# Kernel optimization log

Measured on AMD Instinct MI355X. Metric: run time of the kernel, lower is better.

Reference implementation:

```python
import jax, jax.numpy as jnp
import numpy as np

N, E, G = 10000, 160000, 64     # nodes, edges, graphs in batch
T, F_IN, F_OUT, L = 5, 75, 15, 4  # towers, per-tower in (divide_input=False), per-tower out, conv layers
AVG_DEG_LOG = float(np.log(17.0))  # stand-in for PyG histogram stat (source deg=zeros -> NaN)
BN_EPS = 1e-5
STD_EPS = 1e-5


def _u(key, shape):
    fi, fo = shape[-2], shape[-1]
    lim = float(np.sqrt(6.0 / (fi + fo)))
    return jax.random.uniform(key, shape, jnp.float32, -lim, lim)


def setup_inputs():
    key = jax.random.key(0)
    k = iter(jax.random.split(key, 24))
    inp = {}
    inp["x"] = jax.random.randint(next(k), (N, 2), 0, 21)
    inp["edge_index"] = jax.random.randint(next(k), (2, E), 0, N)
    inp["edge_attr"] = jax.random.randint(next(k), (E, 2), 0, 4)
    inp["batch"] = jnp.sort(jax.random.randint(next(k), (N,), 0, G))
    inp["node_emb"] = jax.random.normal(next(k), (21, 75), jnp.float32)
    inp["edge_emb"] = jax.random.normal(next(k), (4, 25), jnp.float32)
    inp["pre_lin_W"] = _u(next(k), (150, 75)); inp["pre_lin_b"] = jnp.zeros((75,), jnp.float32)
    inp["edge_enc_W"] = _u(next(k), (L, 50, F_IN)); inp["edge_enc_b"] = jnp.zeros((L, F_IN), jnp.float32)
    inp["pre_W"] = _u(next(k), (L, T, 3 * F_IN, F_IN)); inp["pre_b"] = jnp.zeros((L, T, F_IN), jnp.float32)
    inp["post_W"] = _u(next(k), (L, T, 13 * F_IN, F_OUT)); inp["post_b"] = jnp.zeros((L, T, F_OUT), jnp.float32)
    inp["lin_W"] = _u(next(k), (L, T * F_OUT, 75)); inp["lin_b"] = jnp.zeros((L, 75), jnp.float32)
    inp["bn_g"] = jnp.ones((L, 75), jnp.float32); inp["bn_b"] = jnp.zeros((L, 75), jnp.float32)
    inp["mlp_W1"] = _u(next(k), (75, 50)); inp["mlp_b1"] = jnp.zeros((50,), jnp.float32)
    inp["mlp_W2"] = _u(next(k), (50, 25)); inp["mlp_b2"] = jnp.zeros((25,), jnp.float32)
    inp["mlp_W3"] = _u(next(k), (25, 1)); inp["mlp_b3"] = jnp.zeros((1,), jnp.float32)
    return inp


def _forward(x, edge_index, edge_attr, batch, node_emb, edge_emb, pre_lin_W, pre_lin_b,
             edge_enc_W, edge_enc_b, pre_W, pre_b, post_W, post_b, lin_W, lin_b,
             bn_g, bn_b, mlp_W1, mlp_b1, mlp_W2, mlp_b2, mlp_W3, mlp_b3):
    # node / edge embeddings -> features
    h = node_emb[x].reshape(N, 150) @ pre_lin_W + pre_lin_b          # [N,75]
    ea = edge_emb[edge_attr].reshape(E, 50)                           # [E,50]
    src, dst = edge_index[0], edge_index[1]  # messages flow src -> dst (x_j=src, x_i=dst)

    cnt = jax.ops.segment_sum(jnp.ones((E,), jnp.float32), dst, num_segments=N)  # in-degree [N]
    deg = jnp.maximum(cnt, 1.0)[:, None, None]
    log_deg = jnp.log(jnp.maximum(cnt, 1.0) + 1.0)[:, None, None]
    amp = log_deg / AVG_DEG_LOG
    att = AVG_DEG_LOG / log_deg
    has = (cnt > 0)[:, None, None]

    for l in range(L):
        e = ea @ edge_enc_W[l] + edge_enc_b[l]                        # [E,75]
        m_in = jnp.concatenate([h[dst], h[src], e], axis=-1)          # [E,225]
        msgs = jnp.einsum('ec,tcf->etf', m_in, pre_W[l]) + pre_b[l]   # [E,T,75]
        s = jax.ops.segment_sum(msgs, dst, num_segments=N)
        mean = s / deg
        mean_sq = jax.ops.segment_sum(msgs * msgs, dst, num_segments=N) / deg
        std = jnp.sqrt(jax.nn.relu(mean_sq - mean * mean) + STD_EPS)
        mn = jnp.where(has, jax.ops.segment_min(msgs, dst, num_segments=N), 0.0)
        mx = jnp.where(has, jax.ops.segment_max(msgs, dst, num_segments=N), 0.0)
        agg = jnp.concatenate([mean, mn, mx, std], axis=-1)           # [N,T,300]
        scaled = jnp.concatenate([agg, agg * amp, agg * att], axis=-1)  # [N,T,900]
        out = jnp.concatenate([jnp.broadcast_to(h[:, None, :], (N, T, F_IN)), scaled], axis=-1)  # [N,T,975]
        post = jnp.einsum('ntc,tcf->ntf', out, post_W[l]) + post_b[l]  # [N,T,15]
        hc = post.reshape(N, T * F_OUT) @ lin_W[l] + lin_b[l]          # [N,75]
        mu = hc.mean(axis=0)
        var = hc.var(axis=0)  # biased, matches BatchNorm1d training mode
        h = jax.nn.relu((hc - mu) / jnp.sqrt(var + BN_EPS) * bn_g[l] + bn_b[l])

    g = jax.ops.segment_sum(h, batch, num_segments=G)                 # global_add_pool [G,75]
    g = jax.nn.relu(g @ mlp_W1 + mlp_b1)
    g = jax.nn.relu(g @ mlp_W2 + mlp_b2)
    return g @ mlp_W3 + mlp_b3                                        # [G,1]


def reference(x, edge_index, edge_attr, batch, node_emb, edge_emb, pre_lin_W, pre_lin_b,
              edge_enc_W, edge_enc_b, pre_W, pre_b, post_W, post_b, lin_W, lin_b,
              bn_g, bn_b, mlp_W1, mlp_b1, mlp_W2, mlp_b2, mlp_W3, mlp_b3):
    return _forward(x, edge_index, edge_attr, batch, node_emb, edge_emb, pre_lin_W, pre_lin_b,
                    edge_enc_W, edge_enc_b, pre_W, pre_b, post_W, post_b, lin_W, lin_b,
                    bn_g, bn_b, mlp_W1, mlp_b1, mlp_W2, mlp_b2, mlp_W3, mlp_b3)
```

## Files before the change

kernel.cpp:

```cpp
#include <hip/hip_runtime.h>
#include <hip/hip_bf16.h>
#include <math.h>

#define NN 10000
#define NE 160000
#define NG 64
#define NT 5
#define NL 4
#define ADL 2.833213344056216f

#define OFF_H      0
#define OFF_HC     750000
#define OFF_P      1500000
#define OFF_Q      5250000
#define OFF_AGG    9000000
#define OFF_RLUT4  16500000
#define OFF_INVDEG 24006000
#define OFF_AMP    24016000
#define OFF_ATT    24026000
#define OFF_STATS  24036000
#define OFF_GPOOL  24040000
#define OFF_INT    24118960

typedef __attribute__((ext_vector_type(2))) unsigned int uv2;

__device__ __forceinline__ float bf2f(__hip_bfloat16 v){ return __bfloat162float(v); }

__global__ void k_zero_cnt(int* cnt){
    int i = blockIdx.x*256 + threadIdx.x;
    if (i < NN) cnt[i] = 0;
}

__global__ __launch_bounds__(256) void k_h0(const int* __restrict__ x,
        const float* __restrict__ node_emb, const float* __restrict__ plW,
        const float* __restrict__ plb, float* __restrict__ h){
    __shared__ float s_emb[21*75];
    __shared__ float s_W[150*75];
    __shared__ float s_b[75];
    int tid = threadIdx.x;
    for (int i = tid; i < 21*75; i += 256) s_emb[i] = node_emb[i];
    for (int i = tid; i < 150*75; i += 256) s_W[i] = plW[i];
    if (tid < 75) s_b[tid] = plb[tid];
    __syncthreads();
    for (int out = blockIdx.x*256 + tid; out < NN*75; out += gridDim.x*256){
        int n = out / 75, f = out - n*75;
        int x0 = x[2*n], x1 = x[2*n+1];
        float acc = s_b[f];
        const float* e0 = s_emb + x0*75;
        const float* e1 = s_emb + x1*75;
        #pragma unroll 5
        for (int k = 0; k < 75; k++)
            acc += e0[k]*s_W[k*75+f] + e1[k]*s_W[(75+k)*75+f];
        h[out] = acc;
    }
}

__global__ void k_hist(const int* __restrict__ ei, int* __restrict__ cnt){
    int e = blockIdx.x*256 + threadIdx.x;
    if (e < NE) atomicAdd(&cnt[ei[NE + e]], 1);
}

__global__ __launch_bounds__(1024) void k_scan(const int* __restrict__ cnt,
        int* __restrict__ eoff, float* __restrict__ invdeg,
        float* __restrict__ amp, float* __restrict__ att,
        int* __restrict__ cursor){
    __shared__ int wsum[16];
    int tid = threadIdx.x;
    int base = tid*10;
    int v[10];
    int s = 0;
    #pragma unroll
    for (int i = 0; i < 10; i++){
        int n = base + i;
        int c = (n < NN) ? cnt[n] : 0;
        v[i] = s;
        s += c;
    }
    int lane = tid & 63;
    int wave = tid >> 6;
    int inc = s;
    #pragma unroll
    for (int off = 1; off < 64; off <<= 1){
        int t = __shfl_up(inc, off);
        if (lane >= off) inc += t;
    }
    if (lane == 63) wsum[wave] = inc;
    __syncthreads();
    if (tid == 0){
        int acc = 0;
        #pragma unroll
        for (int w = 0; w < 16; w++){ int t = wsum[w]; wsum[w] = acc; acc += t; }
        eoff[0] = 0;
    }
    __syncthreads();
    int ex = inc - s + wsum[wave];
    #pragma unroll
    for (int i = 0; i < 10; i++){
        int n = base + i;
        if (n < NN){
            int c = cnt[n];
            int start = ex + v[i];
            eoff[n+1] = start + c;
            cursor[n] = start;
            float cf = (float)c;
            float dg = cf < 1.f ? 1.f : cf;
            invdeg[n] = 1.f / dg;
            float ld = logf(dg + 1.f);
            amp[n] = ld / ADL;
            att[n] = ADL / ld;
        }
    }
}

__global__ void k_scatter(const int* __restrict__ ei, const int* __restrict__ ea,
        int* __restrict__ cursor, int* __restrict__ esrc, int* __restrict__ ecombo){
    int e = blockIdx.x*256 + threadIdx.x;
    if (e >= NE) return;
    int src = ei[e], dst = ei[NE + e];
    int pos = atomicAdd(&cursor[dst], 1);
    esrc[pos] = src;
    ecombo[pos] = ea[2*e]*4 + ea[2*e+1];
}

__global__ __launch_bounds__(384) void k_rlut4(
        const float* __restrict__ preW, const float* __restrict__ preb,
        const float* __restrict__ edge_emb, const float* __restrict__ encW,
        const float* __restrict__ encb, float* __restrict__ rlut_all){
    __shared__ float smem[10675];
    int tid = threadIdx.x;
    int t = blockIdx.x;
    int l = blockIdx.y;
    float* s_encW = smem;
    float* s_ev   = smem + 3750;
    float* s_wc   = smem + 4950;
    float* s_ee   = smem + 10575;
    for (int i = tid; i < 3750; i += 384) s_encW[i] = encW[(size_t)l*3750 + i];
    for (int i = tid; i < 100; i += 384) s_ee[i] = edge_emb[i];
    const float* wcsrc = preW + (((size_t)(l*NT + t))*225 + 150)*75;
    for (int i = tid; i < 5625; i += 384) s_wc[i] = wcsrc[i];
    __syncthreads();
    for (int task = tid; task < 1200; task += 384){
        int b = task/75, m = task - 75*b;
        int a0 = b >> 2, a1 = b & 3;
        float s = encb[l*75 + m];
        for (int k = 0; k < 25; k++)
            s += s_ee[a0*25+k]*s_encW[k*75+m] + s_ee[a1*25+k]*s_encW[(25+k)*75+m];
        s_ev[task] = s;
    }
    __syncthreads();
    for (int task = tid; task < 1200; task += 384){
        int b = task/75, f = task - 75*b;
        float r = preb[((size_t)l*NT + t)*75 + f];
        const float* ev = s_ev + b*75;
        #pragma unroll 5
        for (int m = 0; m < 75; m++) r += ev[m]*s_wc[m*75 + f];
        rlut_all[(size_t)l*6000 + b*375 + t*75 + f] = r;
    }
}

__global__ __launch_bounds__(256, 4) void k_pq(float* __restrict__ h,
        const float* __restrict__ hc, const float* __restrict__ bng,
        const float* __restrict__ bnb,
        const float* __restrict__ preW,
        int l, __hip_bfloat16* __restrict__ P, __hip_bfloat16* __restrict__ Q,
        const float* __restrict__ stats_all){
    __shared__ float s_h[64*76];
    __shared__ float s_w[76*64];
    int tid = threadIdx.x;
    int base_n = blockIdx.x*64;
    int tx = tid & 15;
    int ty = tid >> 4;

    if (l == 0){
        for (int idx = tid; idx < 64*76; idx += 256){
            int i = idx/76, m = idx - 76*i;
            int n = base_n + i;
            s_h[idx] = (m < 75 && n < NN) ? h[(size_t)n*75 + m] : 0.f;
        }
    } else {
        const float* stats_rd = stats_all + ((l + 1) & 1)*192;
        int lp = l - 1;
        for (int idx = tid; idx < 64*76; idx += 256){
            int i = idx/76, m = idx - 76*i;
            int n = base_n + i;
            float v = 0.f;
            if (m < 75 && n < NN){
                float mu = stats_rd[m]*(1.0f/NN);
                float var = stats_rd[75+m]*(1.0f/NN) - mu*mu;
                float inv = rsqrtf(var + 1e-5f);
                v = (hc[(size_t)n*75 + m] - mu)*inv*bng[lp*75+m] + bnb[lp*75+m];
                v = v > 0.f ? v : 0.f;
                if (blockIdx.y == 0) h[(size_t)n*75 + m] = v;
            }
            s_h[idx] = v;
        }
    }

    for (int half = 0; half < 2; half++){
        int base_c = blockIdx.y*128 + half*64;
        if (half){
            __syncthreads();
        }
        for (int idx = tid; idx < 76*64; idx += 256){
            int k = idx >> 6, c = idx & 63;
            int col = base_c + c;
            float v = 0.f;
            if (k < 75 && col < 750){
                int cc2 = col < 375 ? col : col - 375;
                int t = cc2/75, f = cc2 - t*75;
                int ro = col < 375 ? 0 : 75;
                v = preW[(((size_t)(l*NT + t))*225 + ro + k)*75 + f];
            }
            s_w[idx] = v;
        }
        __syncthreads();

        float acc[4][4] = {};
        const float* hrow = s_h + (ty*4)*76;
        const float* wrow = s_w + tx*4;
        for (int k4 = 0; k4 < 76; k4 += 4){
            float4 hv[4], wv[4];
            #pragma unroll
            for (int r = 0; r < 4; r++)
                hv[r] = *(const float4*)(hrow + r*76 + k4);
            #pragma unroll
            for (int kk = 0; kk < 4; kk++)
                wv[kk] = *(const float4*)(wrow + (k4+kk)*64);
            #pragma unroll
            for (int r = 0; r < 4; r++){
                float h0 = hv[r].x, h1 = hv[r].y, h2 = hv[r].z, h3 = hv[r].w;
                acc[r][0] += h0*wv[0].x + h1*wv[1].x + h2*wv[2].x + h3*wv[3].x;
                acc[r][1] += h0*wv[0].y + h1*wv[1].y + h2*wv[2].y + h3*wv[3].y;
                acc[r][2] += h0*wv[0].z + h1*wv[1].z + h2*wv[2].z + h3*wv[3].z;
                acc[r][3] += h0*wv[0].w + h1*wv[1].w + h2*wv[2].w + h3*wv[3].w;
            }
        }

        #pragma unroll
        for (int r = 0; r < 4; r++){
            int n = base_n + ty*4 + r;
            if (n >= NN) continue;
            #pragma unroll
            for (int cc = 0; cc < 4; cc++){
                int c = base_c + tx*4 + cc;
                if (c >= 750) continue;
                __hip_bfloat16 v = __float2bfloat16(acc[r][cc]);
                if (c < 375) P[(size_t)n*375 + c] = v;
                else         Q[(size_t)n*375 + (c - 375)] = v;
            }
        }
    }
}

__global__ __launch_bounds__(64) void k_agg(const __hip_bfloat16* __restrict__ P,
        const __hip_bfloat16* __restrict__ Q, const float* __restrict__ Rlut,
        const int* __restrict__ eoff, const int* __restrict__ esrc,
        const int* __restrict__ ecombo, const float* __restrict__ invdeg,
        __hip_bfloat16* __restrict__ agg, float* __restrict__ stats_zero){
    int n = blockIdx.y;
    int j = blockIdx.x*64 + threadIdx.x;
    if (blockIdx.x == 0 && n == 0){
        for (int i = threadIdx.x; i < 150; i += 64) stats_zero[i] = 0.f;
    }
    if (j >= 375) return;
    int lo = eoff[n], hi = eoff[n+1];
    float p = bf2f(P[(size_t)n*375 + j]);
    float sum = 0.f, sq = 0.f, mn = 3.4e38f, mx = -3.4e38f;
    int e = lo;
    for (; e + 8 <= hi; e += 8){
        int s0 = esrc[e],   s1 = esrc[e+1], s2 = esrc[e+2], s3 = esrc[e+3];
        int s4 = esrc[e+4], s5 = esrc[e+5], s6 = esrc[e+6], s7 = esrc[e+7];
        int c0 = ecombo[e],   c1 = ecombo[e+1], c2 = ecombo[e+2], c3 = ecombo[e+3];
        int c4 = ecombo[e+4], c5 = ecombo[e+5], c6 = ecombo[e+6], c7 = ecombo[e+7];
        float q0 = bf2f(Q[(size_t)s0*375 + j]);
        float q1 = bf2f(Q[(size_t)s1*375 + j]);
        float q2 = bf2f(Q[(size_t)s2*375 + j]);
        float q3 = bf2f(Q[(size_t)s3*375 + j]);
        float q4 = bf2f(Q[(size_t)s4*375 + j]);
        float q5 = bf2f(Q[(size_t)s5*375 + j]);
        float q6 = bf2f(Q[(size_t)s6*375 + j]);
        float q7 = bf2f(Q[(size_t)s7*375 + j]);
        float r0 = Rlut[c0*375 + j], r1 = Rlut[c1*375 + j];
        float r2 = Rlut[c2*375 + j], r3 = Rlut[c3*375 + j];
        float r4 = Rlut[c4*375 + j], r5 = Rlut[c5*375 + j];
        float r6 = Rlut[c6*375 + j], r7 = Rlut[c7*375 + j];
        float m0 = p + q0 + r0, m1 = p + q1 + r1;
        float m2 = p + q2 + r2, m3 = p + q3 + r3;
        float m4 = p + q4 + r4, m5 = p + q5 + r5;
        float m6 = p + q6 + r6, m7 = p + q7 + r7;
        sum += (m0 + m1 + m2 + m3) + (m4 + m5 + m6 + m7);
        sq  += (m0*m0 + m1*m1 + m2*m2 + m3*m3) + (m4*m4 + m5*m5 + m6*m6 + m7*m7);
        mn = fminf(mn, fminf(fminf(fminf(m0,m1), fminf(m2,m3)),
                             fminf(fminf(m4,m5), fminf(m6,m7))));
        mx = fmaxf(mx, fmaxf(fmaxf(fmaxf(m0,m1), fmaxf(m2,m3)),
                             fmaxf(fmaxf(m4,m5), fmaxf(m6,m7))));
    }
    for (; e < hi; e++){
        int s = esrc[e], cm = ecombo[e];
        float m = p + bf2f(Q[(size_t)s*375 + j]) + Rlut[cm*375 + j];
        sum += m; sq += m*m;
        mn = fminf(mn, m); mx = fmaxf(mx, m);
    }
    float id = invdeg[n];
    bool has = hi > lo;
    float mean = sum*id;
    float msq  = sq*id;
    float var = msq - mean*mean; var = var > 0.f ? var : 0.f;
    float sd = sqrtf(var + 1e-5f);
    float mnv = has ? mn : 0.f;
    float mxv = has ? mx : 0.f;
    int t = j/75, f = j - 75*t;
    __hip_bfloat16* a = agg + ((size_t)n*NT + t)*300;
    a[f]      = __float2bfloat16(mean);
    a[75+f]   = __float2bfloat16(mnv);
    a[150+f]  = __float2bfloat16(mxv);
    a[225+f]  = __float2bfloat16(sd);
}

#define KB2 50
__global__ __launch_bounds__(256, 6) void k_post(const float* __restrict__ h,
        const __hip_bfloat16* __restrict__ agg, const float* __restrict__ postW,
        const float* __restrict__ postb, const float* __restrict__ amp,
        const float* __restrict__ att, int l, __hip_bfloat16* __restrict__ postbase){
    __shared__ float s_w[3*KB2*16];
    __shared__ unsigned short s_a[128*52];
    int t = blockIdx.y;
    int z = blockIdx.z;
    int nbase = blockIdx.x*128;
    int tid = threadIdx.x;
    int fg  = (tid & 3)*4;
    int sub = tid >> 2;
    const float* Wt = postW + ((size_t)(l*NT + t))*975*15;

    if (z == 0){
        for (int idx = tid; idx < 75*16; idx += 256){
            int c = idx >> 4, f = idx & 15;
            s_w[idx] = (f < 15) ? Wt[c*15 + f] : 0.f;
        }
        __syncthreads();
        float a1[2][4] = {};
        const float* hrow[2];
        #pragma unroll
        for (int j = 0; j < 2; j++){
            int n = nbase + sub + 64*j;
            hrow[j] = h + (size_t)(n < NN ? n : 0)*75;
        }
        #pragma unroll 3
        for (int k = 0; k < 75; k++){
            const float4 w1 = *(const float4*)&s_w[k*16 + fg];
            #pragma unroll
            for (int j = 0; j < 2; j++){
                float v = hrow[j][k];
                a1[j][0] += v*w1.x; a1[j][1] += v*w1.y;
                a1[j][2] += v*w1.z; a1[j][3] += v*w1.w;
            }
        }
        const float* pb = postb + (l*NT + t)*15;
        #pragma unroll
        for (int j = 0; j < 2; j++){
            int n = nbase + sub + 64*j;
            if (n >= NN) continue;
            __hip_bfloat16* dst = postbase + (size_t)n*75 + t*15;
            #pragma unroll
            for (int f = 0; f < 4; f++)
                if (fg + f < 15) dst[fg + f] = __float2bfloat16(a1[j][f] + pb[fg + f]);
        }
        return;
    }

    int kbeg = (z-1)*KB2;
    for (int idx = tid; idx < 3*KB2*16; idx += 256){
        int vrow = idx / (KB2*16);
        int rem = idx - vrow*(KB2*16);
        int c = rem >> 4, f = rem & 15;
        s_w[idx] = (f < 15) ? Wt[(75 + vrow*300 + kbeg + c)*15 + f] : 0.f;
    }
    {
        const unsigned short* asrc = (const unsigned short*)agg;
        for (int idx = tid; idx < 128*25; idx += 256){
            int i = idx/25, w = idx - 25*i;
            int n = nbase + i;
            unsigned int u = 0;
            if (n < NN)
                u = *(const unsigned int*)(asrc + (size_t)n*1500 + t*300 + kbeg + 2*w);
            *(unsigned int*)&s_a[i*52 + 2*w] = u;
        }
    }
    __syncthreads();

    float a1[2][4] = {}, a2[2][4] = {}, a3[2][4] = {};
    const unsigned short* ap0 = s_a + sub*52;
    #pragma unroll 2
    for (int k4 = 0; k4 < 48; k4 += 4){
        uv2 ua[2];
        #pragma unroll
        for (int j = 0; j < 2; j++)
            ua[j] = *(const uv2*)(ap0 + j*(64*52) + k4);
        #pragma unroll
        for (int kk = 0; kk < 4; kk++){
            int k = k4 + kk;
            const float4 w1 = *(const float4*)&s_w[k*16 + fg];
            const float4 w2 = *(const float4*)&s_w[(KB2 + k)*16 + fg];
            const float4 w3 = *(const float4*)&s_w[(2*KB2 + k)*16 + fg];
            #pragma unroll
            for (int j = 0; j < 2; j++){
                unsigned int bits = (kk < 2) ? ua[j].x : ua[j].y;
                float v = __uint_as_float((kk & 1) ? (bits & 0xffff0000u)
                                                   : (bits << 16));
                a1[j][0] += v*w1.x; a1[j][1] += v*w1.y;
                a1[j][2] += v*w1.z; a1[j][3] += v*w1.w;
                a2[j][0] += v*w2.x; a2[j][1] += v*w2.y;
                a2[j][2] += v*w2.z; a2[j][3] += v*w2.w;
                a3[j][0] += v*w3.x; a3[j][1] += v*w3.y;
                a3[j][2] += v*w3.z; a3[j][3] += v*w3.w;
            }
        }
    }
    {
        unsigned int ut[2];
        #pragma unroll
        for (int j = 0; j < 2; j++)
            ut[j] = *(const unsigned int*)(ap0 + j*(64*52) + 48);
        #pragma unroll
        for (int kk = 0; kk < 2; kk++){
            int k = 48 + kk;
            const float4 w1 = *(const float4*)&s_w[k*16 + fg];
            const float4 w2 = *(const float4*)&s_w[(KB2 + k)*16 + fg];
            const float4 w3 = *(const float4*)&s_w[(2*KB2 + k)*16 + fg];
            #pragma unroll
            for (int j = 0; j < 2; j++){
                float v = __uint_as_float((kk & 1) ? (ut[j] & 0xffff0000u)
                                                   : (ut[j] << 16));
                a1[j][0] += v*w1.x; a1[j][1] += v*w1.y;
                a1[j][2] += v*w1.z; a1[j][3] += v*w1.w;
                a2[j][0] += v*w2.x; a2[j][1] += v*w2.y;
                a2[j][2] += v*w2.z; a2[j][3] += v*w2.w;
                a3[j][0] += v*w3.x; a3[j][1] += v*w3.y;
                a3[j][2] += v*w3.z; a3[j][3] += v*w3.w;
            }
        }
    }
    __hip_bfloat16* postv = postbase + (size_t)z*750000;
    #pragma unroll
    for (int j = 0; j < 2; j++){
        int n = nbase + sub + 64*j;
        if (n >= NN) continue;
        float am = amp[n], at = att[n];
        __hip_bfloat16* dst = postv + (size_t)n*75 + t*15;
        #pragma unroll
        for (int f = 0; f < 4; f++)
            if (fg + f < 15)
                dst[fg + f] = __float2bfloat16(a1[j][f] + am*a2[j][f] + at*a3[j][f]);
    }
}

__global__ __launch_bounds__(256) void k_lin(const __hip_bfloat16* __restrict__ postbase,
        const float* __restrict__ linW, const float* __restrict__ linb,
        int l, float* __restrict__ hc, float* __restrict__ stats_all){
    __shared__ float p_l[32*75];
    __shared__ float w_l[75*75];
    __shared__ float hc_l[32*75];
    int tid = threadIdx.x;
    int base = blockIdx.x*32;
    for (int i = tid; i < 75*75; i += 256) w_l[i] = linW[(size_t)l*5625 + i];
    for (int i = tid; i < 32*75; i += 256){
        int n = base + i/75;
        size_t idx = (size_t)base*75 + i;
        float v = 0.f;
        if (n < NN){
            #pragma unroll
            for (int z = 0; z < 7; z++) v += bf2f(postbase[idx + (size_t)z*750000]);
        }
        p_l[i] = v;
    }
    __syncthreads();
    for (int task = tid; task < 2400; task += 256){
        int i = task/75, o = task - 75*i;
        float s = linb[l*75 + o];
        const float* pl = p_l + i*75;
        #pragma unroll 5
        for (int j = 0; j < 75; j++) s += pl[j]*w_l[j*75 + o];
        hc_l[task] = s;
        if (base + i < NN) hc[(size_t)(base+i)*75 + o] = s;
    }
    __syncthreads();
    if (tid < 75){
        float* stats_wr = stats_all + (l & 1)*192;
        int nv = NN - base; if (nv > 32) nv = 32;
        float s1 = 0.f, s2 = 0.f;
        for (int i = 0; i < nv; i++){
            float v = hc_l[i*75 + tid];
            s1 += v; s2 += v*v;
        }
        atomicAdd(&stats_wr[tid], s1);
        atomicAdd(&stats_wr[75+tid], s2);
    }
}

__global__ void k_bnapply(const float* __restrict__ hc, const float* __restrict__ stats,
        const float* __restrict__ bng, const float* __restrict__ bnb, int l,
        float* __restrict__ h){
    int idx = blockIdx.x*256 + threadIdx.x;
    if (idx >= NN*75) return;
    int col = idx % 75;
    float mu = stats[col]*(1.0f/NN);
    float var = stats[75+col]*(1.0f/NN) - mu*mu;
    float inv = rsqrtf(var + 1e-5f);
    float v = (hc[idx] - mu)*inv*bng[l*75+col] + bnb[l*75+col];
    h[idx] = v > 0.f ? v : 0.f;
}

__global__ __launch_bounds__(256) void k_pool(const float* __restrict__ h,
        const int* __restrict__ batch, float* __restrict__ gpool){
    int g = blockIdx.x, tid = threadIdx.x;
    int lo = 0, hi = NN;
    while (lo < hi){ int mid = (lo+hi)>>1; if (batch[mid] < g) lo = mid+1; else hi = mid; }
    int start = lo;
    lo = start; hi = NN;
    while (lo < hi){ int mid = (lo+hi)>>1; if (batch[mid] < g+1) lo = mid+1; else hi = mid; }
    int end = lo;
    __shared__ float red[225];
    if (tid < 225){
        int col = tid % 75, rep = tid / 75;
        float acc = 0.f;
        for (int i = start + rep; i < end; i += 3) acc += h[(size_t)i*75 + col];
        red[tid] = acc;
    }
    __syncthreads();
    if (tid < 75) gpool[g*75 + tid] = red[tid] + red[75+tid] + red[150+tid];
}

__global__ __launch_bounds__(256) void k_mlp(const float* __restrict__ gpool,
        const float* __restrict__ W1, const float* __restrict__ b1,
        const float* __restrict__ W2, const float* __restrict__ b2,
        const float* __restrict__ W3, const float* __restrict__ b3,
        float* __restrict__ out){
    __shared__ float w1[75*50];
    __shared__ float w2[50*25];
    __shared__ float gp[8*75];
    __shared__ float t1[8*50];
    __shared__ float t2[8*25];
    int tid = threadIdx.x;
    int gbase = blockIdx.x*8;
    for (int i = tid; i < 75*50; i += 256) w1[i] = W1[i];
    for (int i = tid; i < 50*25; i += 256) w2[i] = W2[i];
    for (int i = tid; i < 8*75; i += 256) gp[i] = gpool[gbase*75 + i];
    __syncthreads();
    for (int task = tid; task < 8*50; task += 256){
        int g = task/50, j = task - 50*g;
        float s = b1[j];
        const float* gv = gp + g*75;
        #pragma unroll 5
        for (int k = 0; k < 75; k++) s += gv[k]*w1[k*50+j];
        t1[task] = s > 0.f ? s : 0.f;
    }
    __syncthreads();
    for (int task = tid; task < 8*25; task += 256){
        int g = task/25, j = task - 25*g;
        float s = b2[j];
        const float* tv = t1 + g*50;
        #pragma unroll 5
        for (int k = 0; k < 50; k++) s += tv[k]*w2[k*25+j];
        t2[task] = s > 0.f ? s : 0.f;
    }
    __syncthreads();
    if (tid < 8){
        float s = b3[0];
        const float* tv = t2 + tid*25;
        #pragma unroll
        for (int k = 0; k < 25; k++) s += tv[k]*W3[k];
        out[gbase + tid] = s;
    }
}

extern "C" void kernel_launch(void* const* d_in, const int* in_sizes, int n_in,
                              void* d_out, int out_size, void* d_ws, size_t ws_size,
                              hipStream_t stream){
    const int* x          = (const int*)d_in[0];
    const int* edge_index = (const int*)d_in[1];
    const int* edge_attr  = (const int*)d_in[2];
    const int* batch      = (const int*)d_in[3];
    const float* node_emb = (const float*)d_in[4];
    const float* edge_emb = (const float*)d_in[5];
    const float* pre_lin_W= (const float*)d_in[6];
    const float* pre_lin_b= (const float*)d_in[7];
    const float* encW     = (const float*)d_in[8];
    const float* encb     = (const float*)d_in[9];
    const float* preW     = (const float*)d_in[10];
    const float* preb     = (const float*)d_in[11];
    const float* postW    = (const float*)d_in[12];
    const float* postb    = (const float*)d_in[13];
    const float* linW     = (const float*)d_in[14];
    const float* linb     = (const float*)d_in[15];
    const float* bng      = (const float*)d_in[16];
    const float* bnb      = (const float*)d_in[17];
    const float* mlpW1    = (const float*)d_in[18];
    const float* mlpb1    = (const float*)d_in[19];
    const float* mlpW2    = (const float*)d_in[20];
    const float* mlpb2    = (const float*)d_in[21];
    const float* mlpW3    = (const float*)d_in[22];
    const float* mlpb3    = (const float*)d_in[23];

    float* ws = (float*)d_ws;
    float* h      = ws + OFF_H;
    float* hc     = ws + OFF_HC;
    __hip_bfloat16* P = (__hip_bfloat16*)(ws + OFF_P);
    __hip_bfloat16* Q = (__hip_bfloat16*)(ws + OFF_Q);
    __hip_bfloat16* agg = (__hip_bfloat16*)(ws + OFF_AGG);
    float* rlut4  = ws + OFF_RLUT4;
    float* invdeg = ws + OFF_INVDEG;
    float* amp    = ws + OFF_AMP;
    float* att    = ws + OFF_ATT;
    float* stats  = ws + OFF_STATS;
    float* gpool  = ws + OFF_GPOOL;
    __hip_bfloat16* postbase = (__hip_bfloat16*)(ws + OFF_P);
    int* iw     = (int*)(ws + OFF_INT);
    int* cnt    = iw;
    int* eoff   = cnt + NN;
    int* cursor = eoff + NN + 2;
    int* esrc   = cursor + NN;
    int* ecombo = esrc + NE;

    k_zero_cnt<<<40, 256, 0, stream>>>(cnt);
    k_rlut4<<<dim3(5, 4), 384, 0, stream>>>(preW, preb, edge_emb, encW, encb, rlut4);
    k_h0<<<640, 256, 0, stream>>>(x, node_emb, pre_lin_W, pre_lin_b, h);
    k_hist<<<625, 256, 0, stream>>>(edge_index, cnt);
    k_scan<<<1, 1024, 0, stream>>>(cnt, eoff, invdeg, amp, att, cursor);
    k_scatter<<<625, 256, 0, stream>>>(edge_index, edge_attr, cursor, esrc, ecombo);

    for (int l = 0; l < NL; l++){
        k_pq<<<dim3(157, 6), 256, 0, stream>>>(h, hc, bng, bnb, preW, l, P, Q, stats);
        k_agg<<<dim3(6, NN), 64, 0, stream>>>(P, Q, rlut4 + (size_t)l*6000,
                                              eoff, esrc, ecombo, invdeg, agg,
                                              stats + (l & 1)*192);
        k_post<<<dim3(79, 5, 7), 256, 0, stream>>>(h, agg, postW, postb, amp, att, l, postbase);
        k_lin<<<313, 256, 0, stream>>>(postbase, linW, linb, l, hc, stats);
    }

    k_bnapply<<<2930, 256, 0, stream>>>(hc, stats + ((NL-1)&1)*192, bng, bnb, NL-1, h);
    k_pool<<<NG, 256, 0, stream>>>(h, batch, gpool);
    k_mlp<<<8, 256, 0, stream>>>(gpool, mlpW1, mlpb1, mlpW2, mlpb2, mlpW3, mlpb3, (float*)d_out);
}
```

Baseline: 786.0 us.

## Accumulate all post-tower K-chunks in one block instead of split-K partials

k_post previously split the 975-wide reduction across 7 z-blocks, each writing a bf16 partial that k_lin then summed. Now each block loops over all six aggregation chunks plus the h chunk itself, keeps the sum in registers and writes one bf16 result. Rows per block drop from 128 to 64, and k_lin reads a single buffer. This removes six partial writes and reads per layer and the bf16 rounding of each partial, but cuts parallelism to 785 blocks that each run serially through six chunks with barriers.

```diff
diff --git a/kernel.cpp b/kernel.cpp
--- a/kernel.cpp
+++ b/kernel.cpp
@@ -318,143 +318,110 @@
 }
 
 #define KB2 50
-__global__ __launch_bounds__(256, 6) void k_post(const float* __restrict__ h,
+__global__ __launch_bounds__(256, 8) void k_post(const float* __restrict__ h,
         const __hip_bfloat16* __restrict__ agg, const float* __restrict__ postW,
         const float* __restrict__ postb, const float* __restrict__ amp,
-        const float* __restrict__ att, int l, __hip_bfloat16* __restrict__ postbase){
+        const float* __restrict__ att, int l, __hip_bfloat16* __restrict__ post){
     __shared__ float s_w[3*KB2*16];
-    __shared__ unsigned short s_a[128*52];
+    __shared__ unsigned short s_a[64*52];
     int t = blockIdx.y;
-    int z = blockIdx.z;
-    int nbase = blockIdx.x*128;
+    int nbase = blockIdx.x*64;
     int tid = threadIdx.x;
     int fg  = (tid & 3)*4;
     int sub = tid >> 2;
+    int n = nbase + sub;
+    int nc = (n < NN) ? n : 0;
     const float* Wt = postW + ((size_t)(l*NT + t))*975*15;
 
-    if (z == 0){
-        for (int idx = tid; idx < 75*16; idx += 256){
-            int c = idx >> 4, f = idx & 15;
-            s_w[idx] = (f < 15) ? Wt[c*15 + f] : 0.f;
-        }
-        __syncthreads();
-        float a1[2][4] = {};
-        const float* hrow[2];
-        #pragma unroll
-        for (int j = 0; j < 2; j++){
-            int n = nbase + sub + 64*j;
-            hrow[j] = h + (size_t)(n < NN ? n : 0)*75;
-        }
+    float zacc[4] = {};
+
+    for (int idx = tid; idx < 75*16; idx += 256){
+        int c = idx >> 4, f = idx & 15;
+        s_w[idx] = (f < 15) ? Wt[c*15 + f] : 0.f;
+    }
+    __syncthreads();
+    {
+        const float* hrow = h + (size_t)nc*75;
         #pragma unroll 3
         for (int k = 0; k < 75; k++){
             const float4 w1 = *(const float4*)&s_w[k*16 + fg];
+            float v = hrow[k];
+            zacc[0] += v*w1.x; zacc[1] += v*w1.y;
+            zacc[2] += v*w1.z; zacc[3] += v*w1.w;
+        }
+    }
+
+    float am = amp[nc], at = att[nc];
+    const unsigned short* asrc = (const unsigned short*)agg;
+
+    for (int z = 1; z <= 6; z++){
+        int kbeg = (z-1)*KB2;
+        __syncthreads();
+        for (int idx = tid; idx < 3*KB2*16; idx += 256){
+            int vrow = idx / (KB2*16);
+            int rem = idx - vrow*(KB2*16);
+            int c = rem >> 4, f = rem & 15;
+            s_w[idx] = (f < 15) ? Wt[(75 + vrow*300 + kbeg + c)*15 + f] : 0.f;
+        }
+        for (int idx = tid; idx < 64*25; idx += 256){
+            int i = idx/25, w = idx - 25*i;
+            int nn2 = nbase + i;
+            unsigned int u = 0;
+            if (nn2 < NN)
+                u = *(const unsigned int*)(asrc + (size_t)nn2*1500 + t*300 + kbeg + 2*w);
+            *(unsigned int*)&s_a[i*52 + 2*w] = u;
+        }
+        __syncthreads();
+
+        float a1[4] = {}, a2[4] = {}, a3[4] = {};
+        const unsigned short* ap0 = s_a + sub*52;
+        #pragma unroll 2
+        for (int k4 = 0; k4 < 48; k4 += 4){
+            uv2 ua = *(const uv2*)(ap0 + k4);
             #pragma unroll
-            for (int j = 0; j < 2; j++){
-                float v = hrow[j][k];
-                a1[j][0] += v*w1.x; a1[j][1] += v*w1.y;
-                a1[j][2] += v*w1.z; a1[j][3] += v*w1.w;
-            }
-        }
-        const float* pb = postb + (l*NT + t)*15;
-        #pragma unroll
-        for (int j = 0; j < 2; j++){
-            int n = nbase + sub + 64*j;
-            if (n >= NN) continue;
-            __hip_bfloat16* dst = postbase + (size_t)n*75 + t*15;
-            #pragma unroll
-            for (int f = 0; f < 4; f++)
-                if (fg + f < 15) dst[fg + f] = __float2bfloat16(a1[j][f] + pb[fg + f]);
-        }
-        return;
-    }
-
-    int kbeg = (z-1)*KB2;
-    for (int idx = tid; idx < 3*KB2*16; idx += 256){
-        int vrow = idx / (KB2*16);
-        int rem = idx - vrow*(KB2*16);
-        int c = rem >> 4, f = rem & 15;
-        s_w[idx] = (f < 15) ? Wt[(75 + vrow*300 + kbeg + c)*15 + f] : 0.f;
-    }
-    {
-        const unsigned short* asrc = (const unsigned short*)agg;
-        for (int idx = tid; idx < 128*25; idx += 256){
-            int i = idx/25, w = idx - 25*i;
-            int n = nbase + i;
-            unsigned int u = 0;
-            if (n < NN)
-                u = *(const unsigned int*)(asrc + (size_t)n*1500 + t*300 + kbeg + 2*w);
-            *(unsigned int*)&s_a[i*52 + 2*w] = u;
-        }
-    }
-    __syncthreads();
-
-    float a1[2][4] = {}, a2[2][4] = {}, a3[2][4] = {};
-    const unsigned short* ap0 = s_a + sub*52;
-    #pragma unroll 2
-    for (int k4 = 0; k4 < 48; k4 += 4){
-        uv2 ua[2];
-        #pragma unroll
-        for (int j = 0; j < 2; j++)
-            ua[j] = *(const uv2*)(ap0 + j*(64*52) + k4);
-        #pragma unroll
-        for (int kk = 0; kk < 4; kk++){
-            int k = k4 + kk;
-            const float4 w1 = *(const float4*)&s_w[k*16 + fg];
-            const float4 w2 = *(const float4*)&s_w[(KB2 + k)*16 + fg];
-            const float4 w3 = *(const float4*)&s_w[(2*KB2 + k)*16 + fg];
-            #pragma unroll
-            for (int j = 0; j < 2; j++){
-                unsigned int bits = (kk < 2) ? ua[j].x : ua[j].y;
+            for (int kk = 0; kk < 4; kk++){
+                int k = k4 + kk;
+                const float4 w1 = *(const float4*)&s_w[k*16 + fg];
+                const float4 w2 = *(const float4*)&s_w[(KB2 + k)*16 + fg];
+                const float4 w3 = *(const float4*)&s_w[(2*KB2 + k)*16 + fg];
+                unsigned int bits = (kk < 2) ? ua.x : ua.y;
                 float v = __uint_as_float((kk & 1) ? (bits & 0xffff0000u)
                                                    : (bits << 16));
-                a1[j][0] += v*w1.x; a1[j][1] += v*w1.y;
-                a1[j][2] += v*w1.z; a1[j][3] += v*w1.w;
-                a2[j][0] += v*w2.x; a2[j][1] += v*w2.y;
-                a2[j][2] += v*w2.z; a2[j][3] += v*w2.w;
-                a3[j][0] += v*w3.x; a3[j][1] += v*w3.y;
-                a3[j][2] += v*w3.z; a3[j][3] += v*w3.w;
+                a1[0] += v*w1.x; a1[1] += v*w1.y; a1[2] += v*w1.z; a1[3] += v*w1.w;
+                a2[0] += v*w2.x; a2[1] += v*w2.y; a2[2] += v*w2.z; a2[3] += v*w2.w;
+                a3[0] += v*w3.x; a3[1] += v*w3.y; a3[2] += v*w3.z; a3[3] += v*w3.w;
             }
         }
-    }
-    {
-        unsigned int ut[2];
-        #pragma unroll
-        for (int j = 0; j < 2; j++)
-            ut[j] = *(const unsigned int*)(ap0 + j*(64*52) + 48);
-        #pragma unroll
-        for (int kk = 0; kk < 2; kk++){
-            int k = 48 + kk;
-            const float4 w1 = *(const float4*)&s_w[k*16 + fg];
-            const float4 w2 = *(const float4*)&s_w[(KB2 + k)*16 + fg];
-            const float4 w3 = *(const float4*)&s_w[(2*KB2 + k)*16 + fg];
+        {
+            unsigned int ut = *(const unsigned int*)(ap0 + 48);
             #pragma unroll
-            for (int j = 0; j < 2; j++){
-                float v = __uint_as_float((kk & 1) ? (ut[j] & 0xffff0000u)
-                                                   : (ut[j] << 16));
-                a1[j][0] += v*w1.x; a1[j][1] += v*w1.y;
-                a1[j][2] += v*w1.z; a1[j][3] += v*w1.w;
-                a2[j][0] += v*w2.x; a2[j][1] += v*w2.y;
-                a2[j][2] += v*w2.z; a2[j][3] += v*w2.w;
-                a3[j][0] += v*w3.x; a3[j][1] += v*w3.y;
-                a3[j][2] += v*w3.z; a3[j][3] += v*w3.w;
+            for (int kk = 0; kk < 2; kk++){
+                int k = 48 + kk;
+                const float4 w1 = *(const float4*)&s_w[k*16 + fg];
+                const float4 w2 = *(const float4*)&s_w[(KB2 + k)*16 + fg];
+                const float4 w3 = *(const float4*)&s_w[(2*KB2 + k)*16 + fg];
+                float v = __uint_as_float((kk & 1) ? (ut & 0xffff0000u)
+                                                   : (ut << 16));
+                a1[0] += v*w1.x; a1[1] += v*w1.y; a1[2] += v*w1.z; a1[3] += v*w1.w;
+                a2[0] += v*w2.x; a2[1] += v*w2.y; a2[2] += v*w2.z; a2[3] += v*w2.w;
+                a3[0] += v*w3.x; a3[1] += v*w3.y; a3[2] += v*w3.z; a3[3] += v*w3.w;
             }
         }
-    }
-    __hip_bfloat16* postv = postbase + (size_t)z*750000;
-    #pragma unroll
-    for (int j = 0; j < 2; j++){
-        int n = nbase + sub + 64*j;
-        if (n >= NN) continue;
-        float am = amp[n], at = att[n];
-        __hip_bfloat16* dst = postv + (size_t)n*75 + t*15;
         #pragma unroll
         for (int f = 0; f < 4; f++)
-            if (fg + f < 15)
-                dst[fg + f] = __float2bfloat16(a1[j][f] + am*a2[j][f] + at*a3[j][f]);
-    }
-}
-
-__global__ __launch_bounds__(256) void k_lin(const __hip_bfloat16* __restrict__ postbase,
+            zacc[f] += a1[f] + am*a2[f] + at*a3[f];
+    }
+
+    if (n < NN){
+        const float* pb = postb + (l*NT + t)*15;
+        __hip_bfloat16* dst = post + (size_t)n*75 + t*15;
+        #pragma unroll
+        for (int f = 0; f < 4; f++)
+            if (fg + f < 15) dst[fg + f] = __float2bfloat16(zacc[f] + pb[fg + f]);
+    }
+}
+
+__global__ __launch_bounds__(256) void k_lin(const __hip_bfloat16* __restrict__ post,
         const float* __restrict__ linW, const float* __restrict__ linb,
         int l, float* __restrict__ hc, float* __restrict__ stats_all){
     __shared__ float p_l[32*75];
@@ -465,13 +432,7 @@
     for (int i = tid; i < 75*75; i += 256) w_l[i] = linW[(size_t)l*5625 + i];
     for (int i = tid; i < 32*75; i += 256){
         int n = base + i/75;
-        size_t idx = (size_t)base*75 + i;
-        float v = 0.f;
-        if (n < NN){
-            #pragma unroll
-            for (int z = 0; z < 7; z++) v += bf2f(postbase[idx + (size_t)z*750000]);
-        }
-        p_l[i] = v;
+        p_l[i] = (n < NN) ? bf2f(post[(size_t)base*75 + i]) : 0.f;
     }
     __syncthreads();
     for (int task = tid; task < 2400; task += 256){
@@ -613,7 +574,7 @@
     float* att    = ws + OFF_ATT;
     float* stats  = ws + OFF_STATS;
     float* gpool  = ws + OFF_GPOOL;
-    __hip_bfloat16* postbase = (__hip_bfloat16*)(ws + OFF_P);
+    __hip_bfloat16* post = (__hip_bfloat16*)(ws + OFF_P);
     int* iw     = (int*)(ws + OFF_INT);
     int* cnt    = iw;
     int* eoff   = cnt + NN;
@@ -633,8 +594,8 @@
         k_agg<<<dim3(6, NN), 64, 0, stream>>>(P, Q, rlut4 + (size_t)l*6000,
                                               eoff, esrc, ecombo, invdeg, agg,
                                               stats + (l & 1)*192);
-        k_post<<<dim3(79, 5, 7), 256, 0, stream>>>(h, agg, postW, postb, amp, att, l, postbase);
-        k_lin<<<313, 256, 0, stream>>>(postbase, linW, linb, l, hc, stats);
+        k_post<<<dim3(157, 5), 256, 0, stream>>>(h, agg, postW, postb, amp, att, l, post);
+        k_lin<<<313, 256, 0, stream>>>(post, linW, linb, l, hc, stats);
     }
 
     k_bnapply<<<2930, 256, 0, stream>>>(hc, stats + ((NL-1)&1)*192, bng, bnb, NL-1, h);
```

After: 904.1 us. 1.15x slower.

## Process one node per 384-thread block in aggregation with LDS-staged edge lists

Applied to the files above, without the earlier changes.

The aggregation kernel now uses one block of 384 threads per node instead of six 64-thread blocks. The block stages the node's edge source and combo indices in shared memory in chunks of 128, so the index loads are read once rather than six times. The goal is fewer blocks to launch, less redundant index traffic, and one wavefront covering all 375 features. In exchange it adds two barriers per chunk, leaves 9 of 384 threads idle, and cuts the unroll from 8 to 4, which may reduce memory-level parallelism on the gathers.

```diff
diff --git a/kernel.cpp b/kernel.cpp
--- a/kernel.cpp
+++ b/kernel.cpp
@@ -252,55 +252,61 @@
     }
 }
 
-__global__ __launch_bounds__(64) void k_agg(const __hip_bfloat16* __restrict__ P,
+#define ACH 128
+__global__ __launch_bounds__(384) void k_agg(const __hip_bfloat16* __restrict__ P,
         const __hip_bfloat16* __restrict__ Q, const float* __restrict__ Rlut,
         const int* __restrict__ eoff, const int* __restrict__ esrc,
         const int* __restrict__ ecombo, const float* __restrict__ invdeg,
         __hip_bfloat16* __restrict__ agg, float* __restrict__ stats_zero){
-    int n = blockIdx.y;
-    int j = blockIdx.x*64 + threadIdx.x;
-    if (blockIdx.x == 0 && n == 0){
-        for (int i = threadIdx.x; i < 150; i += 64) stats_zero[i] = 0.f;
-    }
-    if (j >= 375) return;
+    __shared__ int s_src[ACH];
+    __shared__ int s_cmb[ACH];
+    int n = blockIdx.x;
+    int tid = threadIdx.x;
+    int j = tid;
+    if (n == 0 && tid < 150) stats_zero[tid] = 0.f;
+
     int lo = eoff[n], hi = eoff[n+1];
-    float p = bf2f(P[(size_t)n*375 + j]);
+    bool act = j < 375;
+    float p = act ? bf2f(P[(size_t)n*375 + j]) : 0.f;
     float sum = 0.f, sq = 0.f, mn = 3.4e38f, mx = -3.4e38f;
-    int e = lo;
-    for (; e + 8 <= hi; e += 8){
-        int s0 = esrc[e],   s1 = esrc[e+1], s2 = esrc[e+2], s3 = esrc[e+3];
-        int s4 = esrc[e+4], s5 = esrc[e+5], s6 = esrc[e+6], s7 = esrc[e+7];
-        int c0 = ecombo[e],   c1 = ecombo[e+1], c2 = ecombo[e+2], c3 = ecombo[e+3];
-        int c4 = ecombo[e+4], c5 = ecombo[e+5], c6 = ecombo[e+6], c7 = ecombo[e+7];
-        float q0 = bf2f(Q[(size_t)s0*375 + j]);
-        float q1 = bf2f(Q[(size_t)s1*375 + j]);
-        float q2 = bf2f(Q[(size_t)s2*375 + j]);
-        float q3 = bf2f(Q[(size_t)s3*375 + j]);
-        float q4 = bf2f(Q[(size_t)s4*375 + j]);
-        float q5 = bf2f(Q[(size_t)s5*375 + j]);
-        float q6 = bf2f(Q[(size_t)s6*375 + j]);
-        float q7 = bf2f(Q[(size_t)s7*375 + j]);
-        float r0 = Rlut[c0*375 + j], r1 = Rlut[c1*375 + j];
-        float r2 = Rlut[c2*375 + j], r3 = Rlut[c3*375 + j];
-        float r4 = Rlut[c4*375 + j], r5 = Rlut[c5*375 + j];
-        float r6 = Rlut[c6*375 + j], r7 = Rlut[c7*375 + j];
-        float m0 = p + q0 + r0, m1 = p + q1 + r1;
-        float m2 = p + q2 + r2, m3 = p + q3 + r3;
-        float m4 = p + q4 + r4, m5 = p + q5 + r5;
-        float m6 = p + q6 + r6, m7 = p + q7 + r7;
-        sum += (m0 + m1 + m2 + m3) + (m4 + m5 + m6 + m7);
-        sq  += (m0*m0 + m1*m1 + m2*m2 + m3*m3) + (m4*m4 + m5*m5 + m6*m6 + m7*m7);
-        mn = fminf(mn, fminf(fminf(fminf(m0,m1), fminf(m2,m3)),
-                             fminf(fminf(m4,m5), fminf(m6,m7))));
-        mx = fmaxf(mx, fmaxf(fmaxf(fmaxf(m0,m1), fmaxf(m2,m3)),
-                             fmaxf(fmaxf(m4,m5), fmaxf(m6,m7))));
-    }
-    for (; e < hi; e++){
-        int s = esrc[e], cm = ecombo[e];
-        float m = p + bf2f(Q[(size_t)s*375 + j]) + Rlut[cm*375 + j];
-        sum += m; sq += m*m;
-        mn = fminf(mn, m); mx = fmaxf(mx, m);
-    }
+
+    for (int base_e = lo; base_e < hi; base_e += ACH){
+        int cnt = hi - base_e; if (cnt > ACH) cnt = ACH;
+        __syncthreads();
+        for (int i = tid; i < cnt; i += 384){
+            s_src[i] = esrc[base_e + i];
+            s_cmb[i] = ecombo[base_e + i];
+        }
+        __syncthreads();
+        if (act){
+            int i = 0;
+            for (; i + 4 <= cnt; i += 4){
+                int s0 = s_src[i],   s1 = s_src[i+1];
+                int s2 = s_src[i+2], s3 = s_src[i+3];
+                int c0 = s_cmb[i],   c1 = s_cmb[i+1];
+                int c2 = s_cmb[i+2], c3 = s_cmb[i+3];
+                float q0 = bf2f(Q[(size_t)s0*375 + j]);
+                float q1 = bf2f(Q[(size_t)s1*375 + j]);
+                float q2 = bf2f(Q[(size_t)s2*375 + j]);
+                float q3 = bf2f(Q[(size_t)s3*375 + j]);
+                float r0 = Rlut[c0*375 + j], r1 = Rlut[c1*375 + j];
+                float r2 = Rlut[c2*375 + j], r3 = Rlut[c3*375 + j];
+                float m0 = p + q0 + r0, m1 = p + q1 + r1;
+                float m2 = p + q2 + r2, m3 = p + q3 + r3;
+                sum += (m0 + m1) + (m2 + m3);
+                sq  += (m0*m0 + m1*m1) + (m2*m2 + m3*m3);
+                mn = fminf(mn, fminf(fminf(m0,m1), fminf(m2,m3)));
+                mx = fmaxf(mx, fmaxf(fmaxf(m0,m1), fmaxf(m2,m3)));
+            }
+            for (; i < cnt; i++){
+                int s = s_src[i], cm = s_cmb[i];
+                float m = p + bf2f(Q[(size_t)s*375 + j]) + Rlut[cm*375 + j];
+                sum += m; sq += m*m;
+                mn = fminf(mn, m); mx = fmaxf(mx, m);
+            }
+        }
+    }
+    if (!act) return;
     float id = invdeg[n];
     bool has = hi > lo;
     float mean = sum*id;
@@ -630,9 +636,9 @@
 
     for (int l = 0; l < NL; l++){
         k_pq<<<dim3(157, 6), 256, 0, stream>>>(h, hc, bng, bnb, preW, l, P, Q, stats);
-        k_agg<<<dim3(6, NN), 64, 0, stream>>>(P, Q, rlut4 + (size_t)l*6000,
-                                              eoff, esrc, ecombo, invdeg, agg,
-                                              stats + (l & 1)*192);
+        k_agg<<<NN, 384, 0, stream>>>(P, Q, rlut4 + (size_t)l*6000,
+                                      eoff, esrc, ecombo, invdeg, agg,
+                                      stats + (l & 1)*192);
         k_post<<<dim3(79, 5, 7), 256, 0, stream>>>(h, agg, postW, postb, amp, att, l, postbase);
         k_lin<<<313, 256, 0, stream>>>(postbase, linW, linb, l, hc, stats);
     }
```

New measurement: 791.9 us. No clear change (+0.7%).
